# Kernel tuning notes

Measured on AMD Instinct MI355X. Metric: run time of the kernel, lower is better.

Reference implementation:

```python
import jax, jax.numpy as jnp
import numpy as np

B, H_, W_, C, HEADS, WS, SR = 4, 56, 56, 256, 8, 3, 4
HD = C // HEADS
N = H_ * W_
LL = WS * WS
PH, PW = H_ // SR, W_ // SR
PL = PH * PW
K_TAB = 2048


def _unfold3(x, H, W):
    # x: (B, C, H, W) -> (B, C, 9, H*W); matches torch nn.Unfold(kernel_size=3, padding=1)
    xp = jnp.pad(x, ((0, 0), (0, 0), (1, 1), (1, 1)))
    pats = jnp.stack([xp[:, :, i:i + H, j:j + W] for i in range(3) for j in range(3)], axis=2)
    return pats.reshape(x.shape[0], x.shape[1], 9, H * W)


def _l2n(x):
    # torch F.normalize(dim=-1) with eps=1e-12
    return x / jnp.maximum(jnp.linalg.norm(x, axis=-1, keepdims=True), 1e-12)


def setup_inputs() -> dict:
    key = jax.random.key(0)
    ks = jax.random.split(key, 24)
    x = jax.random.normal(ks[0], (B, N, C), jnp.float32)
    # padding mask from unfold of ones image (True where window element falls outside)
    ones = np.zeros((H_ + 2, W_ + 2), np.float32)
    ones[1:-1, 1:-1] = 1.0
    pats = np.stack([ones[i:i + H_, j:j + W_] for i in range(3) for j in range(3)], 0).reshape(9, N)
    padding_mask = jnp.asarray((pats == 0).T)  # (N, 9) bool
    local_valid = LL - padding_mask.sum(-1)
    seq_length_scale = jnp.log(local_valid.astype(jnp.float32) + PL)[:, None]  # (N,1)
    relative_pos_index = jax.random.randint(ks[1], (N * PL,), 0, K_TAB)
    relative_coords_table = jax.random.uniform(ks[2], (K_TAB, 2), jnp.float32, -1.0, 1.0)
    w = lambda k, shape: jax.random.normal(k, shape, jnp.float32) * 0.02
    inp = dict(
        x=x, H=H_, W=W_,
        relative_pos_index=relative_pos_index,
        relative_coords_table=relative_coords_table,
        seq_length_scale=seq_length_scale,
        padding_mask=padding_mask,
        q_w=w(ks[3], (C, C)), q_b=jnp.zeros((C,), jnp.float32),
        kv_w=w(ks[4], (2 * C, C)), kv_b=jnp.zeros((2 * C,), jnp.float32),
        sr_w=w(ks[5], (C, C)), sr_b=jnp.zeros((C,), jnp.float32),
        norm_g=jnp.ones((C,), jnp.float32), norm_b=jnp.zeros((C,), jnp.float32),
        cpb1_w=w(ks[6], (512, 2)), cpb1_b=jnp.zeros((512,), jnp.float32),
        cpb2_w=w(ks[7], (HEADS, 512)), cpb2_b=jnp.zeros((HEADS,), jnp.float32),
        temperature=jnp.log(jnp.exp(jnp.ones((HEADS, 1, 1), jnp.float32) / 0.24) - 1.0),
        query_embedding=w(ks[8], (HEADS, 1, HD)),
        rel_pos_bias_local=jax.random.normal(ks[9], (HEADS, LL), jnp.float32) * 0.0004,
        learnable_tokens=w(ks[10], (HEADS, HD, LL)),
        learnable_bias=jnp.zeros((HEADS, 1, LL), jnp.float32),
        proj_w=w(ks[11], (C, C)), proj_b=jnp.zeros((C,), jnp.float32),
    )
    return inp


def reference(x, H, W, relative_pos_index, relative_coords_table, seq_length_scale,
              padding_mask, q_w, q_b, kv_w, kv_b, sr_w, sr_b, norm_g, norm_b,
              cpb1_w, cpb1_b, cpb2_w, cpb2_b, temperature, query_embedding,
              rel_pos_bias_local, learnable_tokens, learnable_bias, proj_w, proj_b):
    Bsz, n, Cd = x.shape
    h, hd, ll = HEADS, HD, LL
    pH, pW = H // SR, W // SR
    pL = pH * pW
    # ----- queries -----
    q = (x @ q_w.T + q_b).reshape(Bsz, n, h, hd).transpose(0, 2, 1, 3)  # (B,h,N,d)
    q_norm = _l2n(q)
    q_scaled = (q_norm + query_embedding) * jax.nn.softplus(temperature) * seq_length_scale
    # ----- local branch: unfolded window KV -----
    kv = x @ kv_w.T + kv_b  # (B,N,2C)
    k_loc, v_loc = jnp.split(kv, 2, axis=-1)
    k_loc = _l2n(k_loc.reshape(Bsz, n, h, hd)).reshape(Bsz, n, Cd)
    kv_img = jnp.concatenate([k_loc, v_loc], -1).transpose(0, 2, 1).reshape(Bsz, 2 * Cd, H, W)
    pats = _unfold3(kv_img, H, W).reshape(Bsz, 2 * h, hd, ll, n).transpose(0, 1, 4, 2, 3)  # (B,2h,N,d,ll)
    k_local, v_local = jnp.split(pats, 2, axis=1)
    attn_local = jnp.einsum('bhnd,bhndl->bhnl', q_scaled, k_local) + rel_pos_bias_local[:, None, :]
    attn_local = jnp.where(padding_mask, -jnp.inf, attn_local)
    # ----- global branch: 1x1 conv -> GELU -> avg pool -> LN -> KV -----
    x_img = x.transpose(0, 2, 1).reshape(Bsz, Cd, H, W)
    x_sr = jax.nn.gelu(jnp.einsum('oc,bchw->bohw', sr_w, x_img) + sr_b[None, :, None, None], approximate=False)
    x_pool = x_sr.reshape(Bsz, Cd, pH, SR, pW, SR).mean(axis=(3, 5)).reshape(Bsz, Cd, pL).transpose(0, 2, 1)
    mu = x_pool.mean(-1, keepdims=True)
    var = x_pool.var(-1, keepdims=True)
    x_pool = (x_pool - mu) / jnp.sqrt(var + 1e-5) * norm_g + norm_b
    kvp = (x_pool @ kv_w.T + kv_b).reshape(Bsz, pL, 2 * h, hd).transpose(0, 2, 1, 3)
    k_pool, v_pool = jnp.split(kvp, 2, axis=1)  # each (B,h,pL,d)
    # CPB-MLP relative position bias (interpolate is identity since test==trained resolution)
    tab = jax.nn.relu(relative_coords_table @ cpb1_w.T + cpb1_b) @ cpb2_w.T + cpb2_b  # (K,h)
    pool_bias = tab.T[:, relative_pos_index].reshape(h, n, pL)
    attn_pool = jnp.einsum('bhnd,bhmd->bhnm', q_scaled, _l2n(k_pool)) + pool_bias
    # ----- joint softmax over [local | pool] -----
    attn = jax.nn.softmax(jnp.concatenate([attn_local, attn_pool], axis=-1), axis=-1)
    a_loc, a_pool = attn[..., :ll], attn[..., ll:]
    w_loc = jnp.einsum('bhnd,hdl->bhnl', q_norm, learnable_tokens) + learnable_bias + a_loc
    x_local = jnp.einsum('bhnl,bhndl->bhnd', w_loc, v_local)
    x_glob = jnp.einsum('bhnm,bhmd->bhnd', a_pool, v_pool)
    out = (x_local + x_glob).transpose(0, 2, 1, 3).reshape(Bsz, n, Cd)
    return out @ proj_w.T + proj_b
```

## Files before the change

### kernel.cpp

```cpp
#include <hip/hip_runtime.h>
#include <hip/hip_bf16.h>
#include <math.h>

#define Bn   4
#define Hh   56
#define Wn   56
#define Cn   256
#define NHn  8
#define HDn  32
#define Nn   3136
#define LLn  9
#define PLn  196
#define PWn  14
#define KTABn 2048
#define Mrows 12544
#define MP   224

#define XCNT   3211264
#define QWOFF  XCNT
#define KVWOFF (QWOFF + 65536)
#define SRWOFF (KVWOFF + 131072)
#define PWOFF  (SRWOFF + 65536)
#define TOTCVT (PWOFF + 65536)

typedef __attribute__((ext_vector_type(8))) short short8v;
typedef __attribute__((ext_vector_type(4))) float float4v;

__device__ __forceinline__ unsigned short f2b(float f) {
  __hip_bfloat16 h = __float2bfloat16(f);
  return *(unsigned short*)&h;
}
__device__ __forceinline__ float b2f(unsigned short u) {
  union { unsigned int i; float f; } x; x.i = ((unsigned int)u) << 16; return x.f;
}
__device__ __forceinline__ void u4_to8f(uint4 u, float* o) {
  o[0]=b2f((unsigned short)(u.x&0xffff)); o[1]=b2f((unsigned short)(u.x>>16));
  o[2]=b2f((unsigned short)(u.y&0xffff)); o[3]=b2f((unsigned short)(u.y>>16));
  o[4]=b2f((unsigned short)(u.z&0xffff)); o[5]=b2f((unsigned short)(u.z>>16));
  o[6]=b2f((unsigned short)(u.w&0xffff)); o[7]=b2f((unsigned short)(u.w>>16));
}
__device__ __forceinline__ void gl_lds16(const unsigned short* g, unsigned short* l) {
  __builtin_amdgcn_global_load_lds(
      (const __attribute__((address_space(1))) unsigned int*)g,
      (__attribute__((address_space(3))) unsigned int*)l, 16, 0, 0);
}

__launch_bounds__(256)
__global__ void cvt5(const float* __restrict__ x, const float* __restrict__ qw,
                     const float* __restrict__ kvw, const float* __restrict__ srw,
                     const float* __restrict__ pw, unsigned short* __restrict__ dst)
{
  const int i = (blockIdx.x * 256 + threadIdx.x) * 4;
  const float* src; int off;
  if      (i < XCNT)   { src = x;   off = 0; }
  else if (i < KVWOFF) { src = qw;  off = QWOFF; }
  else if (i < SRWOFF) { src = kvw; off = KVWOFF; }
  else if (i < PWOFF)  { src = srw; off = SRWOFF; }
  else                 { src = pw;  off = PWOFF; }
  const float4 v = *(const float4*)(src + (i - off));
  ushort4 o2;
  o2.x = f2b(v.x); o2.y = f2b(v.y); o2.z = f2b(v.z); o2.w = f2b(v.w);
  *(ushort4*)(dst + i) = o2;
}

template <int MODE>
__launch_bounds__(512)
__global__ void mgemm(const unsigned short* __restrict__ A,
                      const unsigned short* __restrict__ Wb,
                      const float* __restrict__ b0, const float* __restrict__ b1,
                      const float* __restrict__ b2, void* __restrict__ Cv, int Nc,
                      const float* __restrict__ sls, const float* __restrict__ qe,
                      const float* __restrict__ temp, float* __restrict__ Mq)
{
  __shared__ __align__(16) unsigned char smem[34816];
  unsigned short* As = (unsigned short*)smem;
  unsigned short* Bs = (unsigned short*)(smem + 16384);
  const int t = threadIdx.x;
  const int w = t >> 6, lane = t & 63;
  const int q = lane >> 4, ln = lane & 15;
  int n0, m0;
  if constexpr (MODE == 1) {
    const int hw = blockIdx.x;
    const int wid = (hw & 7) * 98 + (hw >> 3);
    n0 = (wid & 7) * 128; m0 = (wid >> 3) * 128;
  } else {
    const int hw = blockIdx.x;
    const int xcd = hw & 7, idx = hw >> 3;
    const int wid = (xcd < 4 ? xcd * 25 : 100 + (xcd - 4) * 24) + idx;
    n0 = (wid & 1) * 128; m0 = (wid >> 1) * 128;
  }
  const int wm = (w >> 1) * 32, wn = (w & 1) * 64;

  float4v acc[2][4];
  #pragma unroll
  for (int mt = 0; mt < 2; ++mt)
    #pragma unroll
    for (int nt = 0; nt < 4; ++nt)
      acc[mt][nt] = (float4v){0.f, 0.f, 0.f, 0.f};

  for (int k0 = 0; k0 < 256; k0 += 64) {
    #pragma unroll
    for (int j = 0; j < 2; ++j) {
      const int u = t + 512 * j;
      const int r = u >> 3, c = u & 7, sc = c ^ (r & 7);
      gl_lds16(A  + (size_t)(m0 + r) * 256 + k0 + sc * 8, As + u * 8);
      gl_lds16(Wb + (size_t)(n0 + r) * 256 + k0 + sc * 8, Bs + u * 8);
    }
    __syncthreads();
    #pragma unroll
    for (int kk = 0; kk < 2; ++kk) {
      short8v af[2], bfr[4];
      const int cg = kk * 4 + q;
      #pragma unroll
      for (int mt = 0; mt < 2; ++mt) {
        const int r = wm + mt * 16 + ln;
        af[mt] = *(const short8v*)(As + r * 64 + (cg ^ (r & 7)) * 8);
      }
      #pragma unroll
      for (int nt = 0; nt < 4; ++nt) {
        const int r = wn + nt * 16 + ln;
        bfr[nt] = *(const short8v*)(Bs + r * 64 + (cg ^ (r & 7)) * 8);
      }
      #pragma unroll
      for (int mt = 0; mt < 2; ++mt)
        #pragma unroll
        for (int nt = 0; nt < 4; ++nt)
          acc[mt][nt] = __builtin_amdgcn_mfma_f32_16x16x32_bf16(af[mt], bfr[nt], acc[mt][nt], 0, 0, 0);
    }
    __syncthreads();
  }

  if constexpr (MODE == 0) {
    float* C = (float*)Cv;
    float* tileF = (float*)smem;
    float bia[4];
    #pragma unroll
    for (int nt = 0; nt < 4; ++nt) bia[nt] = b0[n0 + wn + nt * 16 + ln];
    #pragma unroll
    for (int half = 0; half < 2; ++half) {
      if ((w >> 2) == half) {
        #pragma unroll
        for (int mt = 0; mt < 2; ++mt)
          #pragma unroll
          for (int r = 0; r < 4; ++r)
            #pragma unroll
            for (int nt = 0; nt < 4; ++nt)
              tileF[(wm - half*64 + mt*16 + q*4 + r) * 132 + wn + nt*16 + ln] = acc[mt][nt][r] + bia[nt];
      }
      __syncthreads();
      #pragma unroll
      for (int j = 0; j < 4; ++j) {
        const int i = j * 512 + t;
        const int row = i >> 5, ch = i & 31;
        float4 v = *(const float4*)(tileF + row * 132 + ch * 4);
        *(float4*)(C + (size_t)(m0 + half * 64 + row) * Nc + n0 + ch * 4) = v;
      }
      __syncthreads();
    }
  } else {
    unsigned short* Cb = (unsigned short*)Cv;
    unsigned short* tileC = (unsigned short*)smem;
    const int seg = n0 >> 8;
    const int h0 = (n0 + wn) >> 5, h1 = h0 + 1;
    float spt0 = 0.f, spt1 = 0.f;
    if (seg == 0) { spt0 = log1pf(__expf(temp[h0])); spt1 = log1pf(__expf(temp[h1])); }
    float bia[4], qev[4];
    #pragma unroll
    for (int nt = 0; nt < 4; ++nt) {
      const int col = n0 + wn + nt * 16 + ln;
      bia[nt] = (seg == 0) ? b0[col] : (seg == 3 ? b2[col - 768] : b1[col - 256]);
      if (seg == 0) qev[nt] = qe[col];
    }
    #pragma unroll
    for (int mt = 0; mt < 2; ++mt) {
      #pragma unroll
      for (int r = 0; r < 4; ++r) {
        const int row = m0 + wm + mt * 16 + q * 4 + r;
        const int lrow = wm + mt * 16 + q * 4 + r;
        float vals[4];
        #pragma unroll
        for (int nt = 0; nt < 4; ++nt) vals[nt] = acc[mt][nt][r] + bia[nt];
        if (seg == 0) {
          float ss0 = vals[0]*vals[0] + vals[1]*vals[1];
          float ss1 = vals[2]*vals[2] + vals[3]*vals[3];
          #pragma unroll
          for (int mk = 1; mk <= 8; mk <<= 1) { ss0 += __shfl_xor(ss0, mk); ss1 += __shfl_xor(ss1, mk); }
          const float i0 = 1.f / fmaxf(sqrtf(ss0), 1e-12f);
          const float i1 = 1.f / fmaxf(sqrtf(ss1), 1e-12f);
          const int nidx = row % Nn, bb = row / Nn;
          const float sl = sls[nidx];
          float qsv[4];
          #pragma unroll
          for (int nt = 0; nt < 4; ++nt) {
            const float inv = (nt < 2) ? i0 : i1;
            const float sp  = (nt < 2) ? spt0 : spt1;
            qsv[nt] = (vals[nt] * inv + qev[nt]) * sp * sl;
          }
          float t0 = qsv[0]*qsv[0] + qsv[1]*qsv[1];
          float t1 = qsv[2]*qsv[2] + qsv[3]*qsv[3];
          #pragma unroll
          for (int mk = 1; mk <= 8; mk <<= 1) { t0 += __shfl_xor(t0, mk); t1 += __shfl_xor(t1, mk); }
          if (ln == 0) {
            Mq[((size_t)(bb * NHn + h0)) * Nn + nidx] = sqrtf(t0);
            Mq[((size_t)(bb * NHn + h1)) * Nn + nidx] = sqrtf(t1);
          }
          #pragma unroll
          for (int nt = 0; nt < 4; ++nt)
            tileC[lrow * 136 + wn + nt*16 + ln] = f2b(qsv[nt]);
        } else if (seg == 1) {
          float ss0 = vals[0]*vals[0] + vals[1]*vals[1];
          float ss1 = vals[2]*vals[2] + vals[3]*vals[3];
          #pragma unroll
          for (int mk = 1; mk <= 8; mk <<= 1) { ss0 += __shfl_xor(ss0, mk); ss1 += __shfl_xor(ss1, mk); }
          const float i0 = 1.f / fmaxf(sqrtf(ss0), 1e-12f);
          const float i1 = 1.f / fmaxf(sqrtf(ss1), 1e-12f);
          #pragma unroll
          for (int nt = 0; nt < 4; ++nt)
            tileC[lrow * 136 + wn + nt*16 + ln] = f2b(vals[nt] * ((nt < 2) ? i0 : i1));
        } else if (seg == 2) {
          #pragma unroll
          for (int nt = 0; nt < 4; ++nt)
            tileC[lrow * 136 + wn + nt*16 + ln] = f2b(vals[nt]);
        } else {
          #pragma unroll
          for (int nt = 0; nt < 4; ++nt) {
            const float v = vals[nt];
            tileC[lrow * 136 + wn + nt*16 + ln] =
              f2b(0.5f * v * (1.0f + erff(v * 0.70710678118654752f)));
          }
        }
      }
    }
    __syncthreads();
    #pragma unroll
    for (int j = 0; j < 4; ++j) {
      const int i = j * 512 + t;
      const int row = i >> 4, ch = i & 15;
      uint4 v = *(const uint4*)(tileC + row * 136 + ch * 8);
      *(uint4*)(Cb + (size_t)(m0 + row) * 1024 + n0 + ch * 8) = v;
    }
  }
}

__launch_bounds__(256)
__global__ void gemm_pp(const float* __restrict__ A, const float* __restrict__ W,
                        const float* __restrict__ bias,
                        unsigned short* __restrict__ kbf,
                        unsigned short* __restrict__ vbf)
{
  __shared__ __align__(16) float As[16][64];
  __shared__ __align__(16) float Ws[16][64];
  const int t  = threadIdx.x;
  const int m0 = blockIdx.y * 64, n0 = blockIdx.x * 64;
  const int lm = t >> 2, lk = (t & 3) << 2;
  const int tx = t & 15, ty = t >> 4;
  float acc[4][4] = {};
  int arow = m0 + lm; if (arow >= Bn*PLn) arow = Bn*PLn - 1;
  const int wrow = n0 + lm;
  for (int k0 = 0; k0 < 256; k0 += 16) {
    float4 av = *(const float4*)(A + (size_t)arow * 256 + k0 + lk);
    As[lk+0][lm] = av.x; As[lk+1][lm] = av.y; As[lk+2][lm] = av.z; As[lk+3][lm] = av.w;
    float4 wv = *(const float4*)(W + (size_t)wrow * 256 + k0 + lk);
    Ws[lk+0][lm] = wv.x; Ws[lk+1][lm] = wv.y; Ws[lk+2][lm] = wv.z; Ws[lk+3][lm] = wv.w;
    __syncthreads();
    #pragma unroll
    for (int k = 0; k < 16; ++k) {
      float4 a = *(const float4*)&As[k][ty << 2];
      float4 w = *(const float4*)&Ws[k][tx << 2];
      acc[0][0] += a.x*w.x; acc[0][1] += a.x*w.y; acc[0][2] += a.x*w.z; acc[0][3] += a.x*w.w;
      acc[1][0] += a.y*w.x; acc[1][1] += a.y*w.y; acc[1][2] += a.y*w.z; acc[1][3] += a.y*w.w;
      acc[2][0] += a.z*w.x; acc[2][1] += a.z*w.y; acc[2][2] += a.z*w.z; acc[2][3] += a.z*w.w;
      acc[3][0] += a.w*w.x; acc[3][1] += a.w*w.y; acc[3][2] += a.w*w.z; acc[3][3] += a.w*w.w;
    }
    __syncthreads();
  }
  const bool is_k = (n0 < 256);
  const int cb = is_k ? n0 : n0 - 256;
  const int head = (cb + tx * 4) >> 5;
  const int d0   = (cb + tx * 4) & 31;
  float vals[4][4];
  #pragma unroll
  for (int i = 0; i < 4; ++i)
    #pragma unroll
    for (int j = 0; j < 4; ++j)
      vals[i][j] = acc[i][j] + bias[n0 + tx * 4 + j];

  if (is_k) {
    #pragma unroll
    for (int i = 0; i < 4; ++i) {
      const int row = m0 + (ty << 2) + i;
      float ss = vals[i][0]*vals[i][0] + vals[i][1]*vals[i][1]
               + vals[i][2]*vals[i][2] + vals[i][3]*vals[i][3];
      ss += __shfl_xor(ss, 1); ss += __shfl_xor(ss, 2); ss += __shfl_xor(ss, 4);
      if (row < Bn*PLn) {
        const float inv = 1.f / fmaxf(sqrtf(ss), 1e-12f);
        const int bb = row / PLn, m = row - bb * PLn;
        const int bh = bb * NHn + head;
        ushort4 o;
        o.x = f2b(vals[i][0] * inv); o.y = f2b(vals[i][1] * inv);
        o.z = f2b(vals[i][2] * inv); o.w = f2b(vals[i][3] * inv);
        *(ushort4*)(kbf + ((size_t)bh * MP + m) * HDn + d0) = o;
      }
    }
  } else {
    const int row0 = m0 + (ty << 2);
    if (row0 < Bn*PLn) {
      const int bb = row0 / PLn, m = row0 - bb * PLn;
      const int bh = bb * NHn + head;
      #pragma unroll
      for (int j = 0; j < 4; ++j) {
        ushort4 o;
        o.x = f2b(vals[0][j]); o.y = f2b(vals[1][j]);
        o.z = f2b(vals[2][j]); o.w = f2b(vals[3][j]);
        *(ushort4*)(vbf + ((size_t)bh * 32 + d0 + j) * MP + m) = o;
      }
    }
  }
}

__launch_bounds__(256)
__global__ void pool_ln_k(const unsigned short* __restrict__ fused, float* __restrict__ pln,
                          const float* __restrict__ g, const float* __restrict__ bb)
{
  const int blk = blockIdx.x;
  const int b = blk / PLn, pc = blk % PLn;
  const int pi = pc / PWn, pj = pc % PWn;
  const int c = threadIdx.x;
  float s = 0.f;
  #pragma unroll
  for (int r = 0; r < 4; ++r)
    #pragma unroll
    for (int cc = 0; cc < 4; ++cc) {
      const int n = (pi*4 + r) * Wn + pj*4 + cc;
      s += b2f(fused[((size_t)b * Nn + n) * 1024 + 768 + c]);
    }
  s *= (1.f/16.f);
  float sum = s, sq = s*s;
  #pragma unroll
  for (int m = 32; m >= 1; m >>= 1) { sum += __shfl_xor(sum, m); sq += __shfl_xor(sq, m); }
  __shared__ float sm[8];
  const int lane = c & 63, wid = c >> 6;
  if (lane == 0) { sm[wid] = sum; sm[4+wid] = sq; }
  __syncthreads();
  const float tot  = sm[0]+sm[1]+sm[2]+sm[3];
  const float totq = sm[4]+sm[5]+sm[6]+sm[7];
  const float mu  = tot * (1.f/256.f);
  const float var = totq * (1.f/256.f) - mu*mu;
  pln[(size_t)blk * Cn + c] = (s - mu) / sqrtf(var + 1e-5f) * g[c] + bb[c];
}

__launch_bounds__(64)
__global__ void cpb_k(const float* __restrict__ rct, const float* __restrict__ w1,
                      const float* __restrict__ b1, const float* __restrict__ w2,
                      const float* __restrict__ b2, float* __restrict__ tab)
{
  const int r = blockIdx.x, t = threadIdx.x;
  const float c0 = rct[r*2], c1 = rct[r*2+1];
  float part[8] = {};
  #pragma unroll
  for (int jj = 0; jj < 8; ++jj) {
    const int j = t * 8 + jj;
    float hv = fmaxf(c0 * w1[j*2] + c1 * w1[j*2+1] + b1[j], 0.f);
    #pragma unroll
    for (int h = 0; h < 8; ++h) part[h] += hv * w2[h*512 + j];
  }
  #pragma unroll
  for (int h = 0; h < 8; ++h)
    for (int mm = 32; mm >= 1; mm >>= 1) part[h] += __shfl_xor(part[h], mm);
  if (t < 8) tab[r*8 + t] = part[t] + b2[t];
}

__launch_bounds__(1024)
__global__ void redmax_k(const float* __restrict__ tab, const float* __restrict__ rpb,
                         float* __restrict__ scal,
                         unsigned short* __restrict__ kbf,
                         unsigned short* __restrict__ vbf)
{
  float mx = -1e30f;
  for (int i = threadIdx.x; i < KTABn*NHn; i += 1024) mx = fmaxf(mx, tab[i]);
  if (threadIdx.x < NHn*LLn) mx = fmaxf(mx, rpb[threadIdx.x]);
  #pragma unroll
  for (int m = 32; m >= 1; m >>= 1) mx = fmaxf(mx, __shfl_xor(mx, m));
  __shared__ float sm[16];
  if ((threadIdx.x & 63) == 0) sm[threadIdx.x >> 6] = mx;
  __syncthreads();
  if (threadIdx.x == 0) {
    float m2 = sm[0];
    #pragma unroll
    for (int i = 1; i < 16; ++i) m2 = fmaxf(m2, sm[i]);
    scal[0] = m2;
  }
  for (int i = threadIdx.x; i < 32*112; i += 1024) {
    const int bh = i / 112;
    *(uint4*)(kbf + (size_t)bh * (MP*HDn) + PLn*HDn + (i % 112) * 8) = (uint4){0,0,0,0};
  }
  for (int i = threadIdx.x; i < 1024*7; i += 1024) {
    const int bhd = i / 7;
    *(ushort4*)(vbf + (size_t)bhd * MP + PLn + (i % 7) * 4) = (ushort4){0,0,0,0};
  }
}

__launch_bounds__(256)
__global__ void bias_g2(const int* __restrict__ rpi, const float* __restrict__ tab,
                        unsigned short* __restrict__ bias2)
{
  const int nt = blockIdx.x, h = blockIdx.y;
  const int t = threadIdx.x;
  const int row = t >> 4, ln = t & 15;
  const int n = nt * 16 + row;
  union { uint4 u[2]; unsigned short s[16]; } pk;
  #pragma unroll
  for (int mt = 0; mt < 16; ++mt) {
    const int m = mt * 16 + ln;
    unsigned short v;
    if (mt < 14 && m < PLn) {
      const int idx = rpi[(size_t)n * PLn + m];
      v = f2b(tab[(size_t)idx * NHn + h]);
    } else {
      v = 0xFF80;
    }
    pk.s[mt] = v;
  }
  unsigned short* dst = bias2 + ((((size_t)h * 196 + nt) * 256 + t) << 4);
  *(uint4*)dst = pk.u[0];
  *(uint4*)(dst + 8) = pk.u[1];
}

__launch_bounds__(256, 5)
__global__ void attn_f(const unsigned short* __restrict__ fused,
                       const unsigned short* __restrict__ kbf,
                       const unsigned short* __restrict__ vbf,
                       const unsigned short* __restrict__ bias2,
                       const float* __restrict__ Mq, const float* __restrict__ scal,
                       const float* __restrict__ slsp, const float* __restrict__ temp,
                       const float* __restrict__ qe, const float* __restrict__ lt,
                       const float* __restrict__ lb, const float* __restrict__ rpb,
                       unsigned short* __restrict__ outp)
{
  __shared__ __align__(16) unsigned short sh[16292];
  unsigned short* k_s = sh;
  unsigned short* v_s = sh + 5696;
  float* park = (float*)(sh + 11392);
  float* tabf = (float*)(sh + 15616);
  float* qe_s  = tabf;
  float* lt_s  = tabf + 32;
  float* lb_s  = tabf + 320;
  float* rpb_s = tabf + 329;
  const int t = threadIdx.x;
  const int w = t >> 6, lane = t & 63;
  const int ln = lane & 15, quad = lane >> 4;
  const int hw = blockIdx.x;
  const int wid = (hw & 7) * 196 + (hw >> 3);
  const int tile = wid % 49;
  const int bh = wid / 49;
  const int h = bh & 7, b = bh >> 3;

  const int base_n = tile * 64 - 57;
  for (int i = t; i < 712; i += 256) {
    const int c4 = i & 3;
    int rg = base_n + (i >> 2); rg = rg < 0 ? 0 : (rg > Nn - 1 ? Nn - 1 : rg);
    const unsigned short* src = fused + ((size_t)(b * Nn + rg)) * 1024 + 256 + h * HDn + c4 * 8;
    gl_lds16(src, k_s + i * 8);
    gl_lds16(src + 256, v_s + i * 8);
  }
  if (t < 32) qe_s[t] = qe[h * HDn + t];
  for (int i = t; i < HDn * LLn; i += 256) lt_s[i] = lt[h * HDn * LLn + i];
  if (t < LLn) { lb_s[t] = lb[h * LLn + t]; rpb_s[t] = rpb[h * LLn + t]; }
  __syncthreads();

  const int nb = tile * 64 + w * 16;
  const int nt2 = tile * 4 + w;
  const short8v afrag = *(const short8v*)(fused +
      ((size_t)(b * Nn + nb + ln)) * 1024 + h * HDn + quad * 8);
  float M4[4];
  const float sc = scal[0];
  #pragma unroll
  for (int r = 0; r < 4; ++r) M4[r] = Mq[(size_t)bh * Nn + nb + quad * 4 + r] + sc;

  union U16 { uint4 u[2]; unsigned short s[16]; };
  U16 breg[4];
  #pragma unroll
  for (int r = 0; r < 4; ++r) {
    const unsigned short* bp = bias2 +
        ((((size_t)h * 196 + nt2) * 256 + (quad * 4 + r) * 16 + ln) << 4);
    breg[r].u[0] = *(const uint4*)bp;
    breg[r].u[1] = *(const uint4*)(bp + 8);
  }

  const unsigned short* kg = kbf + (size_t)bh * (MP * HDn);
  const unsigned short* vg = vbf + (size_t)bh * (32 * MP);
  unsigned short* pst = sh + 11392 + w * 1056;

  float4v accO[2];
  accO[0] = (float4v){0.f,0.f,0.f,0.f};
  accO[1] = (float4v){0.f,0.f,0.f,0.f};
  float lsum[4] = {0.f, 0.f, 0.f, 0.f};

  #pragma unroll
  for (int kc = 0; kc < 7; ++kc) {
    #pragma unroll
    for (int mtl = 0; mtl < 2; ++mtl) {
      const int mt = kc * 2 + mtl;
      short8v bfrag = *(const short8v*)(kg + (mt * 16 + ln) * HDn + quad * 8);
      float4v s = __builtin_amdgcn_mfma_f32_16x16x32_bf16(afrag, bfrag,
                                                          (float4v){0.f,0.f,0.f,0.f}, 0, 0, 0);
      #pragma unroll
      for (int r = 0; r < 4; ++r) {
        const float bv = b2f(breg[r].s[mt]);
        const float p = __expf(s[r] + bv - M4[r]);
        const unsigned short pb = f2b(p);
        lsum[r] += b2f(pb);
        pst[(quad * 4 + r) * 40 + mtl * 16 + ln] = pb;
      }
    }
    short8v pa = *(const short8v*)(pst + ln * 40 + quad * 8);
    #pragma unroll
    for (int nt = 0; nt < 2; ++nt) {
      short8v vb = *(const short8v*)(vg + (size_t)(nt * 16 + ln) * MP + kc * 32 + quad * 8);
      accO[nt] = __builtin_amdgcn_mfma_f32_16x16x32_bf16(pa, vb, accO[nt], 0, 0, 0);
    }
  }

  #pragma unroll
  for (int r = 0; r < 4; ++r) {
    #pragma unroll
    for (int mk = 1; mk <= 8; mk <<= 1) lsum[r] += __shfl_xor(lsum[r], mk);
  }

  float* mypark = park + w * 528;
  #pragma unroll
  for (int r = 0; r < 4; ++r) {
    const int row = quad * 4 + r;
    mypark[row * 33 + ln]      = accO[0][r];
    mypark[row * 33 + 16 + ln] = accO[1][r];
    if (ln == 0) mypark[row * 33 + 32] = lsum[r];
  }

  const int nl = t >> 2, dg = t & 3;
  const int n = tile * 64 + nl;
  float qs8[8];
  u4_to8f(*(const uint4*)(fused + ((size_t)(b * Nn + n)) * 1024 + h * HDn + dg * 8), qs8);
  const float M = Mq[(size_t)bh * Nn + n] + sc;
  const float spt = log1pf(__expf(temp[h]));
  const float inv_qs = 1.f / (spt * slsp[n]);

  float acc8[8], ext8[8];
  #pragma unroll
  for (int j = 0; j < 8; ++j) { acc8[j] = 0.f; ext8[j] = 0.f; }
  float l_run = 0.f;
  const int pi = n / Wn, pj = n % Wn;
  const int sb = nl + 57;
  #pragma unroll
  for (int lc = 0; lc < LLn; ++lc) {
    const int ii = pi + lc/3 - 1, jj = pj + (lc%3) - 1;
    if (ii < 0 || ii >= Hh || jj < 0 || jj >= Wn) continue;
    const int slot = sb + (lc/3 - 1) * 56 + (lc%3) - 1;
    float kk8[8], vv8[8];
    u4_to8f(*(const uint4*)(k_s + slot * 32 + dg * 8), kk8);
    u4_to8f(*(const uint4*)(v_s + slot * 32 + dg * 8), vv8);
    float pp = 0.f, ep = 0.f;
    #pragma unroll
    for (int j = 0; j < 8; ++j) {
      pp += qs8[j] * kk8[j];
      ep += (qs8[j] * inv_qs - qe_s[dg*8 + j]) * lt_s[(dg*8 + j) * LLn + lc];
    }
    pp += __shfl_xor(pp, 1); pp += __shfl_xor(pp, 2);
    ep += __shfl_xor(ep, 1); ep += __shfl_xor(ep, 2);
    const float e = ep + lb_s[lc];
    const float p = __expf(pp + rpb_s[lc] - M);
    l_run += p;
    #pragma unroll
    for (int j = 0; j < 8; ++j) { acc8[j] += p * vv8[j]; ext8[j] += e * vv8[j]; }
  }

  const float* pool_r = park + w * 528 + (nl - w * 16) * 33;
  const float l_pool = pool_r[32];
  const float invl = 1.f / (l_run + l_pool);
  uint4 u;
  {
    const float* op = pool_r + dg * 8;
    float o0 = (acc8[0]+op[0])*invl + ext8[0], o1 = (acc8[1]+op[1])*invl + ext8[1];
    float o2 = (acc8[2]+op[2])*invl + ext8[2], o3 = (acc8[3]+op[3])*invl + ext8[3];
    float o4 = (acc8[4]+op[4])*invl + ext8[4], o5 = (acc8[5]+op[5])*invl + ext8[5];
    float o6 = (acc8[6]+op[6])*invl + ext8[6], o7 = (acc8[7]+op[7])*invl + ext8[7];
    u.x = f2b(o0) | ((unsigned int)f2b(o1) << 16);
    u.y = f2b(o2) | ((unsigned int)f2b(o3) << 16);
    u.z = f2b(o4) | ((unsigned int)f2b(o5) << 16);
    u.w = f2b(o6) | ((unsigned int)f2b(o7) << 16);
  }
  *(uint4*)(outp + ((size_t)b * Nn + n) * Cn + h * HDn + dg * 8) = u;
}

extern "C" void kernel_launch(void* const* d_in, const int* in_sizes, int n_in,
                              void* d_out, int out_size, void* d_ws, size_t ws_size,
                              hipStream_t stream)
{
  const float* x    = (const float*)d_in[0];
  const int*   rpi  = (const int*)d_in[3];
  const float* rct  = (const float*)d_in[4];
  const float* sls  = (const float*)d_in[5];
  const float* q_w  = (const float*)d_in[7];
  const float* q_b  = (const float*)d_in[8];
  const float* kv_w = (const float*)d_in[9];
  const float* kv_b = (const float*)d_in[10];
  const float* sr_w = (const float*)d_in[11];
  const float* sr_b = (const float*)d_in[12];
  const float* ng   = (const float*)d_in[13];
  const float* nbta = (const float*)d_in[14];
  const float* c1w  = (const float*)d_in[15];
  const float* c1b  = (const float*)d_in[16];
  const float* c2w  = (const float*)d_in[17];
  const float* c2b  = (const float*)d_in[18];
  const float* temp = (const float*)d_in[19];
  const float* qe   = (const float*)d_in[20];
  const float* rpb  = (const float*)d_in[21];
  const float* lt   = (const float*)d_in[22];
  const float* lb   = (const float*)d_in[23];
  const float* pw   = (const float*)d_in[24];
  const float* pb   = (const float*)d_in[25];

  float* ws = (float*)d_ws;
  size_t o = 0;
  unsigned short* bf = (unsigned short*)(ws + o); o += TOTCVT / 2;
  unsigned short* fused = (unsigned short*)(ws + o); o += (size_t)Mrows * 512;
  float* Mq    = ws + o;  o += (size_t)Bn * NHn * Nn;
  float* pln   = ws + o;  o += (size_t)Bn * PLn * Cn;
  unsigned short* kbf = (unsigned short*)(ws + o); o += (size_t)Bn * NHn * MP * HDn / 2;
  unsigned short* vbf = (unsigned short*)(ws + o); o += (size_t)Bn * NHn * 32 * MP / 2;
  float* tab   = ws + o;  o += (size_t)KTABn * NHn;
  float* scal  = ws + o;  o += 8;
  unsigned short* bias2 = (unsigned short*)(ws + o); o += (size_t)NHn * 196 * 256 * 16 / 2;
  unsigned short* outp  = (unsigned short*)(ws + o); o += (size_t)Mrows * Cn / 2;

  const unsigned short* xbf   = bf;
  const unsigned short* qkvsw = bf + QWOFF;
  const unsigned short* pwbf  = bf + PWOFF;

  cvt5<<<TOTCVT/1024, 256, 0, stream>>>(x, q_w, kv_w, sr_w, pw, bf);
  mgemm<1><<<784, 512, 0, stream>>>(xbf, qkvsw, q_b, kv_b, sr_b, fused, 1024,
                                    sls, qe, temp, Mq);
  pool_ln_k<<<Bn*PLn, 256, 0, stream>>>(fused, pln, ng, nbta);
  gemm_pp<<<dim3(8, 13), 256, 0, stream>>>(pln, kv_w, kv_b, kbf, vbf);
  cpb_k<<<KTABn, 64, 0, stream>>>(rct, c1w, c1b, c2w, c2b, tab);
  redmax_k<<<1, 1024, 0, stream>>>(tab, rpb, scal, kbf, vbf);
  bias_g2<<<dim3(196, NHn), 256, 0, stream>>>(rpi, tab, bias2);
  attn_f<<<1568, 256, 0, stream>>>(fused, kbf, vbf, bias2, Mq, scal,
                                   sls, temp, qe, lt, lb, rpb, outp);
  mgemm<0><<<196, 512, 0, stream>>>(outp, pwbf, pb, pb, pb, (float*)d_out, 256,
                                    nullptr, nullptr, nullptr, nullptr);
}
```

Baseline: 226.5 us.

## Merge small setup kernels into two multi-role launches to cut launch count

The CPB-MLP table computation and the kbf/vbf zero-padding are folded into the bf16 conversion kernel as extra block ranges. Pool+LayerNorm, bias gathering and the global max reduction are merged into one mid kernel. The launch count drops from nine to six, and the tiny single-block redmax kernel no longer runs serially between stages. The max reduction now sits in a single 256-thread block within a grid of 2353, and its reads of tab rely on the earlier cvt_misc launch having finished, which stream ordering provides.

```diff
diff --git a/kernel.cpp b/kernel.cpp
--- a/kernel.cpp
+++ b/kernel.cpp
@@ -22,6 +22,7 @@
 #define SRWOFF (KVWOFF + 131072)
 #define PWOFF  (SRWOFF + 65536)
 #define TOTCVT (PWOFF + 65536)
+#define CVTBLK (TOTCVT/1024)
 
 typedef __attribute__((ext_vector_type(8))) short short8v;
 typedef __attribute__((ext_vector_type(4))) float float4v;
@@ -46,21 +47,55 @@
 }
 
 __launch_bounds__(256)
-__global__ void cvt5(const float* __restrict__ x, const float* __restrict__ qw,
-                     const float* __restrict__ kvw, const float* __restrict__ srw,
-                     const float* __restrict__ pw, unsigned short* __restrict__ dst)
+__global__ void cvt_misc(const float* __restrict__ x, const float* __restrict__ qw,
+                         const float* __restrict__ kvw, const float* __restrict__ srw,
+                         const float* __restrict__ pw, unsigned short* __restrict__ dst,
+                         const float* __restrict__ rct, const float* __restrict__ w1,
+                         const float* __restrict__ b1, const float* __restrict__ w2,
+                         const float* __restrict__ b2c, float* __restrict__ tab,
+                         unsigned short* __restrict__ kbf, unsigned short* __restrict__ vbf)
 {
-  const int i = (blockIdx.x * 256 + threadIdx.x) * 4;
-  const float* src; int off;
-  if      (i < XCNT)   { src = x;   off = 0; }
-  else if (i < KVWOFF) { src = qw;  off = QWOFF; }
-  else if (i < SRWOFF) { src = kvw; off = KVWOFF; }
-  else if (i < PWOFF)  { src = srw; off = SRWOFF; }
-  else                 { src = pw;  off = PWOFF; }
-  const float4 v = *(const float4*)(src + (i - off));
-  ushort4 o2;
-  o2.x = f2b(v.x); o2.y = f2b(v.y); o2.z = f2b(v.z); o2.w = f2b(v.w);
-  *(ushort4*)(dst + i) = o2;
+  const int blk = blockIdx.x;
+  const int t = threadIdx.x;
+  if (blk < CVTBLK) {
+    const int i = (blk * 256 + t) * 4;
+    const float* src; int off;
+    if      (i < XCNT)   { src = x;   off = 0; }
+    else if (i < KVWOFF) { src = qw;  off = QWOFF; }
+    else if (i < SRWOFF) { src = kvw; off = KVWOFF; }
+    else if (i < PWOFF)  { src = srw; off = SRWOFF; }
+    else                 { src = pw;  off = PWOFF; }
+    const float4 v = *(const float4*)(src + (i - off));
+    ushort4 o2;
+    o2.x = f2b(v.x); o2.y = f2b(v.y); o2.z = f2b(v.z); o2.w = f2b(v.w);
+    *(ushort4*)(dst + i) = o2;
+  } else if (blk < CVTBLK + 512) {
+    const int w = t >> 6, lane = t & 63;
+    const int r = (blk - CVTBLK) * 4 + w;
+    const float c0 = rct[r*2], c1 = rct[r*2+1];
+    float part[8] = {};
+    #pragma unroll
+    for (int jj = 0; jj < 8; ++jj) {
+      const int j = lane * 8 + jj;
+      float hv = fmaxf(c0 * w1[j*2] + c1 * w1[j*2+1] + b1[j], 0.f);
+      #pragma unroll
+      for (int h = 0; h < 8; ++h) part[h] += hv * w2[h*512 + j];
+    }
+    #pragma unroll
+    for (int h = 0; h < 8; ++h)
+      for (int mm = 32; mm >= 1; mm >>= 1) part[h] += __shfl_xor(part[h], mm);
+    if (lane < 8) tab[r*8 + lane] = part[lane] + b2c[lane];
+  } else {
+    const int i = (blk - (CVTBLK + 512)) * 256 + t;
+    for (int j = i; j < 32*112; j += 4096) {
+      const int bh = j / 112;
+      *(uint4*)(kbf + (size_t)bh * (MP*HDn) + PLn*HDn + (j % 112) * 8) = (uint4){0,0,0,0};
+    }
+    for (int j = i; j < 1024*7; j += 4096) {
+      const int bhd = j / 7;
+      *(ushort4*)(vbf + (size_t)bhd * MP + PLn + (j % 7) * 4) = (ushort4){0,0,0,0};
+    }
+  }
 }
 
 template <int MODE>
@@ -243,6 +278,73 @@
 }
 
 __launch_bounds__(256)
+__global__ void mid_k(const unsigned short* __restrict__ fused, float* __restrict__ pln,
+                      const float* __restrict__ g, const float* __restrict__ bbln,
+                      const int* __restrict__ rpi, const float* __restrict__ tab,
+                      unsigned short* __restrict__ bias2,
+                      const float* __restrict__ rpb, float* __restrict__ scal)
+{
+  const int blk = blockIdx.x;
+  const int t = threadIdx.x;
+  __shared__ float sm[8];
+  if (blk < 784) {
+    const int b = blk / PLn, pc = blk % PLn;
+    const int pi = pc / PWn, pj = pc % PWn;
+    const int c = t;
+    float s = 0.f;
+    #pragma unroll
+    for (int r = 0; r < 4; ++r)
+      #pragma unroll
+      for (int cc = 0; cc < 4; ++cc) {
+        const int n = (pi*4 + r) * Wn + pj*4 + cc;
+        s += b2f(fused[((size_t)b * Nn + n) * 1024 + 768 + c]);
+      }
+    s *= (1.f/16.f);
+    float sum = s, sq = s*s;
+    #pragma unroll
+    for (int m = 32; m >= 1; m >>= 1) { sum += __shfl_xor(sum, m); sq += __shfl_xor(sq, m); }
+    const int lane = c & 63, wid = c >> 6;
+    if (lane == 0) { sm[wid] = sum; sm[4+wid] = sq; }
+    __syncthreads();
+    const float tot  = sm[0]+sm[1]+sm[2]+sm[3];
+    const float totq = sm[4]+sm[5]+sm[6]+sm[7];
+    const float mu  = tot * (1.f/256.f);
+    const float var = totq * (1.f/256.f) - mu*mu;
+    pln[(size_t)blk * Cn + c] = (s - mu) / sqrtf(var + 1e-5f) * g[c] + bbln[c];
+  } else if (blk < 2352) {
+    const int idx = blk - 784;
+    const int nt = idx % 196, h = idx / 196;
+    const int row = t >> 4, ln = t & 15;
+    const int n = nt * 16 + row;
+    union { uint4 u[2]; unsigned short s[16]; } pk;
+    #pragma unroll
+    for (int mt = 0; mt < 16; ++mt) {
+      const int m = mt * 16 + ln;
+      unsigned short v;
+      if (mt < 14 && m < PLn) {
+        const int ix = rpi[(size_t)n * PLn + m];
+        v = f2b(tab[(size_t)ix * NHn + h]);
+      } else {
+        v = 0xFF80;
+      }
+      pk.s[mt] = v;
+    }
+    unsigned short* dst = bias2 + ((((size_t)h * 196 + nt) * 256 + t) << 4);
+    *(uint4*)dst = pk.u[0];
+    *(uint4*)(dst + 8) = pk.u[1];
+  } else {
+    float mx = -1e30f;
+    for (int i = t; i < KTABn*NHn; i += 256) mx = fmaxf(mx, tab[i]);
+    if (t < NHn*LLn) mx = fmaxf(mx, rpb[t]);
+    #pragma unroll
+    for (int m = 32; m >= 1; m >>= 1) mx = fmaxf(mx, __shfl_xor(mx, m));
+    if ((t & 63) == 0) sm[t >> 6] = mx;
+    __syncthreads();
+    if (t == 0) scal[0] = fmaxf(fmaxf(sm[0], sm[1]), fmaxf(sm[2], sm[3]));
+  }
+}
+
+__launch_bounds__(256)
 __global__ void gemm_pp(const float* __restrict__ A, const float* __restrict__ W,
                         const float* __restrict__ bias,
                         unsigned short* __restrict__ kbf,
@@ -316,114 +418,6 @@
       }
     }
   }
-}
-
-__launch_bounds__(256)
-__global__ void pool_ln_k(const unsigned short* __restrict__ fused, float* __restrict__ pln,
-                          const float* __restrict__ g, const float* __restrict__ bb)
-{
-  const int blk = blockIdx.x;
-  const int b = blk / PLn, pc = blk % PLn;
-  const int pi = pc / PWn, pj = pc % PWn;
-  const int c = threadIdx.x;
-  float s = 0.f;
-  #pragma unroll
-  for (int r = 0; r < 4; ++r)
-    #pragma unroll
-    for (int cc = 0; cc < 4; ++cc) {
-      const int n = (pi*4 + r) * Wn + pj*4 + cc;
-      s += b2f(fused[((size_t)b * Nn + n) * 1024 + 768 + c]);
-    }
-  s *= (1.f/16.f);
-  float sum = s, sq = s*s;
-  #pragma unroll
-  for (int m = 32; m >= 1; m >>= 1) { sum += __shfl_xor(sum, m); sq += __shfl_xor(sq, m); }
-  __shared__ float sm[8];
-  const int lane = c & 63, wid = c >> 6;
-  if (lane == 0) { sm[wid] = sum; sm[4+wid] = sq; }
-  __syncthreads();
-  const float tot  = sm[0]+sm[1]+sm[2]+sm[3];
-  const float totq = sm[4]+sm[5]+sm[6]+sm[7];
-  const float mu  = tot * (1.f/256.f);
-  const float var = totq * (1.f/256.f) - mu*mu;
-  pln[(size_t)blk * Cn + c] = (s - mu) / sqrtf(var + 1e-5f) * g[c] + bb[c];
-}
-
-__launch_bounds__(64)
-__global__ void cpb_k(const float* __restrict__ rct, const float* __restrict__ w1,
-                      const float* __restrict__ b1, const float* __restrict__ w2,
-                      const float* __restrict__ b2, float* __restrict__ tab)
-{
-  const int r = blockIdx.x, t = threadIdx.x;
-  const float c0 = rct[r*2], c1 = rct[r*2+1];
-  float part[8] = {};
-  #pragma unroll
-  for (int jj = 0; jj < 8; ++jj) {
-    const int j = t * 8 + jj;
-    float hv = fmaxf(c0 * w1[j*2] + c1 * w1[j*2+1] + b1[j], 0.f);
-    #pragma unroll
-    for (int h = 0; h < 8; ++h) part[h] += hv * w2[h*512 + j];
-  }
-  #pragma unroll
-  for (int h = 0; h < 8; ++h)
-    for (int mm = 32; mm >= 1; mm >>= 1) part[h] += __shfl_xor(part[h], mm);
-  if (t < 8) tab[r*8 + t] = part[t] + b2[t];
-}
-
-__launch_bounds__(1024)
-__global__ void redmax_k(const float* __restrict__ tab, const float* __restrict__ rpb,
-                         float* __restrict__ scal,
-                         unsigned short* __restrict__ kbf,
-                         unsigned short* __restrict__ vbf)
-{
-  float mx = -1e30f;
-  for (int i = threadIdx.x; i < KTABn*NHn; i += 1024) mx = fmaxf(mx, tab[i]);
-  if (threadIdx.x < NHn*LLn) mx = fmaxf(mx, rpb[threadIdx.x]);
-  #pragma unroll
-  for (int m = 32; m >= 1; m >>= 1) mx = fmaxf(mx, __shfl_xor(mx, m));
-  __shared__ float sm[16];
-  if ((threadIdx.x & 63) == 0) sm[threadIdx.x >> 6] = mx;
-  __syncthreads();
-  if (threadIdx.x == 0) {
-    float m2 = sm[0];
-    #pragma unroll
-    for (int i = 1; i < 16; ++i) m2 = fmaxf(m2, sm[i]);
-    scal[0] = m2;
-  }
-  for (int i = threadIdx.x; i < 32*112; i += 1024) {
-    const int bh = i / 112;
-    *(uint4*)(kbf + (size_t)bh * (MP*HDn) + PLn*HDn + (i % 112) * 8) = (uint4){0,0,0,0};
-  }
-  for (int i = threadIdx.x; i < 1024*7; i += 1024) {
-    const int bhd = i / 7;
-    *(ushort4*)(vbf + (size_t)bhd * MP + PLn + (i % 7) * 4) = (ushort4){0,0,0,0};
-  }
-}
-
-__launch_bounds__(256)
-__global__ void bias_g2(const int* __restrict__ rpi, const float* __restrict__ tab,
-                        unsigned short* __restrict__ bias2)
-{
-  const int nt = blockIdx.x, h = blockIdx.y;
-  const int t = threadIdx.x;
-  const int row = t >> 4, ln = t & 15;
-  const int n = nt * 16 + row;
-  union { uint4 u[2]; unsigned short s[16]; } pk;
-  #pragma unroll
-  for (int mt = 0; mt < 16; ++mt) {
-    const int m = mt * 16 + ln;
-    unsigned short v;
-    if (mt < 14 && m < PLn) {
-      const int idx = rpi[(size_t)n * PLn + m];
-      v = f2b(tab[(size_t)idx * NHn + h]);
-    } else {
-      v = 0xFF80;
-    }
-    pk.s[mt] = v;
-  }
-  unsigned short* dst = bias2 + ((((size_t)h * 196 + nt) * 256 + t) << 4);
-  *(uint4*)dst = pk.u[0];
-  *(uint4*)(dst + 8) = pk.u[1];
 }
 
 __launch_bounds__(256, 5)
@@ -636,14 +630,12 @@
   const unsigned short* qkvsw = bf + QWOFF;
   const unsigned short* pwbf  = bf + PWOFF;
 
-  cvt5<<<TOTCVT/1024, 256, 0, stream>>>(x, q_w, kv_w, sr_w, pw, bf);
+  cvt_misc<<<CVTBLK + 512 + 16, 256, 0, stream>>>(x, q_w, kv_w, sr_w, pw, bf,
+                                                  rct, c1w, c1b, c2w, c2b, tab, kbf, vbf);
   mgemm<1><<<784, 512, 0, stream>>>(xbf, qkvsw, q_b, kv_b, sr_b, fused, 1024,
                                     sls, qe, temp, Mq);
-  pool_ln_k<<<Bn*PLn, 256, 0, stream>>>(fused, pln, ng, nbta);
+  mid_k<<<2353, 256, 0, stream>>>(fused, pln, ng, nbta, rpi, tab, bias2, rpb, scal);
   gemm_pp<<<dim3(8, 13), 256, 0, stream>>>(pln, kv_w, kv_b, kbf, vbf);
-  cpb_k<<<KTABn, 64, 0, stream>>>(rct, c1w, c1b, c2w, c2b, tab);
-  redmax_k<<<1, 1024, 0, stream>>>(tab, rpb, scal, kbf, vbf);
-  bias_g2<<<dim3(196, NHn), 256, 0, stream>>>(rpi, tab, bias2);
   attn_f<<<1568, 256, 0, stream>>>(fused, kbf, vbf, bias2, Mq, scal,
                                    sls, temp, qe, lt, lb, rpb, outp);
   mgemm<0><<<196, 512, 0, stream>>>(outp, pwbf, pb, pb, pb, (float*)d_out, 256,
```

After: 219.2 us, median of 2. -3.2%, faster.
